# Kernel tuning notes

Measured on AMD Instinct MI355X. Metric: run time of the kernel, lower is better.

## Reference

```python
import jax, jax.numpy as jnp
import numpy as np

N = 100_000      # nodes
E = 1_600_000    # edges (no self loops; reference appends them)
G = 1_000        # graphs
FIN = 27         # input node features
HID = 128        # hidden_channels
L = 4            # num_layers
H = 8            # num_heads
B = 4            # num_bases
A = 3            # aggregators: sum, mean, max
FH = HID // H    # per-head out dim
EPS = 1e-5


def setup_inputs() -> dict:
    key = jax.random.key(0)
    ks = jax.random.split(key, 16)
    s = 0.05
    x = jax.random.normal(ks[0], (N, FIN), jnp.float32)
    src = jax.random.randint(ks[1], (E,), 0, N)
    off = jax.random.randint(ks[2], (E,), 1, N)
    dst = (src + off) % N  # guaranteed no self loops
    edge_index = jnp.stack([src, dst]).astype(jnp.int64)
    batch = jnp.sort(jax.random.randint(ks[3], (N,), 0, G)).astype(jnp.int64)
    return {
        "x": x,
        "lin1_w": jax.random.normal(ks[4], (FIN, HID), jnp.float32) * s,
        "lin1_b": jnp.zeros((HID,), jnp.float32),
        "bn1_g": jnp.ones((HID,), jnp.float32),
        "bn1_b": jnp.zeros((HID,), jnp.float32),
        "bases_w": jax.random.normal(ks[5], (L, HID, B * FH), jnp.float32) * s,
        "comb_w": jax.random.normal(ks[6], (L, HID, H * B * A), jnp.float32) * s,
        "comb_b": jnp.zeros((L, H * B * A), jnp.float32),
        "conv_bias": jnp.zeros((L, HID), jnp.float32),
        "bn_g": jnp.ones((L, HID), jnp.float32),
        "bn_b": jnp.zeros((L, HID), jnp.float32),
        "mlp_w1": jax.random.normal(ks[7], (HID, HID // 2), jnp.float32) * s,
        "mbn1_g": jnp.ones((HID // 2,), jnp.float32),
        "mbn1_b": jnp.zeros((HID // 2,), jnp.float32),
        "mlp_w2": jax.random.normal(ks[8], (HID // 2, HID // 4), jnp.float32) * s,
        "mbn2_g": jnp.ones((HID // 4,), jnp.float32),
        "mbn2_b": jnp.zeros((HID // 4,), jnp.float32),
        "mlp_w3": jax.random.normal(ks[9], (HID // 4, 10), jnp.float32) * s,
        "mlp_b3": jnp.zeros((10,), jnp.float32),
        "edge_index": edge_index,
        "batch": batch,
    }


def _bn(h, g, b):
    # BatchNorm1d, training mode (biased batch variance), per-feature over nodes
    mu = jnp.mean(h, axis=0)
    var = jnp.mean((h - mu) ** 2, axis=0)
    return g * (h - mu) * jax.lax.rsqrt(var + EPS) + b


def reference(x, lin1_w, lin1_b, bn1_g, bn1_b, bases_w, comb_w, comb_b,
              conv_bias, bn_g, bn_b, mlp_w1, mbn1_g, mbn1_b, mlp_w2,
              mbn2_g, mbn2_b, mlp_w3, mlp_b3, edge_index, batch):
    # add self loops (inputs contain none, matching remove+add in EGConv)
    loop = jnp.arange(N, dtype=edge_index.dtype)
    src = jnp.concatenate([edge_index[0], loop])
    dst = jnp.concatenate([edge_index[1], loop])

    h = jax.nn.relu(_bn(x @ lin1_w + lin1_b, bn1_g, bn1_b))  # [N, HID]

    ones_e = jnp.ones((src.shape[0], 1), h.dtype)
    deg = jax.ops.segment_sum(ones_e, dst, num_segments=N)  # [N,1], >=1 via self loops

    for l in range(L):
        bases = h @ bases_w[l]                              # [N, B*FH]
        comb = (h @ comb_w[l] + comb_b[l]).reshape(N, H, A * B)
        msg = bases[src]                                    # [E+N, B*FH]
        ssum = jax.ops.segment_sum(msg, dst, num_segments=N)
        smean = ssum / deg
        smax = jax.ops.segment_max(msg, dst, num_segments=N)
        agg = jnp.stack([ssum, smean, smax], axis=1)        # [N, A, B*FH]
        agg = agg.reshape(N, A * B, FH)
        out = jnp.einsum('nhk,nkf->nhf', comb, agg).reshape(N, HID) + conv_bias[l]
        h = h + jax.nn.relu(_bn(out, bn_g[l], bn_b[l]))

    # global mean pool over graphs
    gsum = jax.ops.segment_sum(h, batch, num_segments=G)
    gcnt = jnp.maximum(jax.ops.segment_sum(jnp.ones((N, 1), h.dtype), batch, num_segments=G), 1.0)
    g = gsum / gcnt                                         # [G, HID]

    g = jax.nn.relu(_bn(g @ mlp_w1, mbn1_g, mbn1_b))
    g = jax.nn.relu(_bn(g @ mlp_w2, mbn2_g, mbn2_b))
    return g @ mlp_w3 + mlp_b3                              # [G, 10]
```

## Files before the change

kernel.cpp:

```cpp
#include <hip/hip_runtime.h>

#define EPSV 1e-5f
#define NEGINF -3.402823466e38f
#define NBMAX 1600
#define CHUNK 8192
#define CAP3 6144

typedef short bf16x8 __attribute__((ext_vector_type(8)));
typedef float f32x4 __attribute__((ext_vector_type(4)));

__device__ __forceinline__ unsigned short f2bf(float f) {
    union { float f; unsigned i; } c; c.f = f;
    unsigned r = c.i + 0x7fff + ((c.i >> 16) & 1);
    return (unsigned short)(r >> 16);
}
__device__ __forceinline__ float blo(unsigned u) {
    union { unsigned i; float f; } c; c.i = u << 16; return c.f;
}
__device__ __forceinline__ float bhi(unsigned u) {
    union { unsigned i; float f; } c; c.i = u & 0xffff0000u; return c.f;
}

__global__ void k_lin1(const float* __restrict__ x, const float* __restrict__ w,
                       const float* __restrict__ bvec, float* __restrict__ outb,
                       float* __restrict__ stats, int N)
{
    int l  = threadIdx.x & 63;
    int wv = threadIdx.x >> 6;
    int waveSlots = gridDim.x * 4;
    int trips = (N + waveSlots - 1) / waveSlots;
    float s0 = 0.f, q0 = 0.f, s1 = 0.f, q1 = 0.f;
    for (int it = 0; it < trips; ++it) {
        int n = (it * gridDim.x + blockIdx.x) * 4 + wv;
        if (n < N) {
            const float* xr = x + (size_t)n * 27;
            float a0 = bvec[l], a1 = bvec[64 + l];
            #pragma unroll
            for (int k = 0; k < 27; ++k) {
                float xv = xr[k];
                a0 = fmaf(xv, w[k * 128 + l], a0);
                a1 = fmaf(xv, w[k * 128 + 64 + l], a1);
            }
            outb[(size_t)n * 128 + l] = a0;
            outb[(size_t)n * 128 + 64 + l] = a1;
            s0 += a0; q0 += a0 * a0; s1 += a1; q1 += a1 * a1;
        }
    }
    __shared__ float sred[4][256];
    sred[0][threadIdx.x] = s0; sred[1][threadIdx.x] = q0;
    sred[2][threadIdx.x] = s1; sred[3][threadIdx.x] = q1;
    __syncthreads();
    if (threadIdx.x < 64) {
        int t = threadIdx.x;
        float v0 = sred[0][t] + sred[0][t + 64] + sred[0][t + 128] + sred[0][t + 192];
        float v1 = sred[1][t] + sred[1][t + 64] + sred[1][t + 128] + sred[1][t + 192];
        float v2 = sred[2][t] + sred[2][t + 64] + sred[2][t + 128] + sred[2][t + 192];
        float v3 = sred[3][t] + sred[3][t + 64] + sred[3][t + 128] + sred[3][t + 192];
        atomicAdd(stats + t, v0);
        atomicAdd(stats + 128 + t, v1);
        atomicAdd(stats + 64 + t, v2);
        atomicAdd(stats + 192 + t, v3);
    }
}

__global__ __launch_bounds__(256)
void k_p1_hist(const int* __restrict__ dst, int* __restrict__ bcnt,
               int E, int NB, int shift)
{
    __shared__ int hist[NBMAX];
    for (int i = threadIdx.x; i < NB; i += 256) hist[i] = 0;
    __syncthreads();
    int stride = gridDim.x * 256;
    for (int e = blockIdx.x * 256 + threadIdx.x; e < E; e += stride)
        atomicAdd(&hist[dst[e] >> shift], 1);
    __syncthreads();
    for (int i = threadIdx.x; i < NB; i += 256)
        if (hist[i]) atomicAdd(bcnt + i, hist[i]);
}

__global__ void k_scan1(const int* __restrict__ cnt, int* __restrict__ rowptr,
                        int* __restrict__ bsum, int N)
{
    __shared__ int sb[256];
    int i = blockIdx.x * 256 + threadIdx.x;
    int v = (i < N) ? cnt[i] : 0;
    sb[threadIdx.x] = v;
    __syncthreads();
    for (int ofs = 1; ofs < 256; ofs <<= 1) {
        int u = (threadIdx.x >= ofs) ? sb[threadIdx.x - ofs] : 0;
        __syncthreads();
        sb[threadIdx.x] += u;
        __syncthreads();
    }
    if (i < N) rowptr[i] = sb[threadIdx.x] - v;
    if (threadIdx.x == 255) bsum[blockIdx.x] = sb[255];
}

__global__ void k_scan2(int* __restrict__ bs, int nb)
{
    __shared__ int sb[512];
    int t = threadIdx.x;
    int v = (t < nb) ? bs[t] : 0;
    sb[t] = v;
    __syncthreads();
    for (int ofs = 1; ofs < 512; ofs <<= 1) {
        int u = (t >= ofs) ? sb[t - ofs] : 0;
        __syncthreads();
        sb[t] += u;
        __syncthreads();
    }
    bs[t] = sb[t] - v;
}

__global__ void k_scan3(int* __restrict__ rowptr, const int* __restrict__ bsum,
                        int N, int E)
{
    int i = blockIdx.x * blockDim.x + threadIdx.x;
    if (i < N) rowptr[i] += bsum[i >> 8];
    if (i == 0) rowptr[N] = E;
}

__global__ __launch_bounds__(256)
void k_p2_scatter(const int* __restrict__ src, const int* __restrict__ dst,
                  const int* __restrict__ bbase, int* __restrict__ bcur0,
                  uint2* __restrict__ bucketed, int E, int NB, int shift)
{
    __shared__ uint2 ebuf[CHUNK];
    __shared__ int hist[NBMAX];
    __shared__ int cur[NBMAX];
    __shared__ int wtmp[256];
    int tid = threadIdx.x;
    int c0 = blockIdx.x * CHUNK;
    int cc = min(CHUNK, E - c0);
    if (cc <= 0) return;

    for (int i = tid; i < NB; i += 256) hist[i] = 0;
    __syncthreads();
    for (int i = tid; i < cc; i += 256)
        atomicAdd(&hist[dst[c0 + i] >> shift], 1);
    __syncthreads();
    int per = (NB + 255) / 256;
    int beg = tid * per, end = min(beg + per, NB);
    int s = 0;
    for (int i = beg; i < end; ++i) s += hist[i];
    wtmp[tid] = s;
    __syncthreads();
    for (int ofs = 1; ofs < 256; ofs <<= 1) {
        int u = (tid >= ofs) ? wtmp[tid - ofs] : 0;
        __syncthreads();
        wtmp[tid] += u;
        __syncthreads();
    }
    int run = wtmp[tid] - s;
    for (int i = beg; i < end; ++i) { cur[i] = run; run += hist[i]; }
    __syncthreads();
    for (int i = tid; i < cc; i += 256) {
        int sv = src[c0 + i], dv = dst[c0 + i];
        int b = dv >> shift;
        int pos = atomicAdd(&cur[b], 1);
        ebuf[pos] = make_uint2((unsigned)sv, (unsigned)dv);
    }
    __syncthreads();
    for (int b = tid; b < NB; b += 256) {
        int c = hist[b];
        if (c > 0) {
            int lb = cur[b] - c;
            int gb = bbase[b] + atomicAdd(&bcur0[b], c);
            hist[b] = gb - lb;
        }
    }
    __syncthreads();
    for (int i = tid; i < cc; i += 256) {
        uint2 u = ebuf[i];
        int b = (int)(u.y >> shift);
        bucketed[hist[b] + i] = u;
    }
}

__global__ __launch_bounds__(256)
void k_p3_csr(const uint2* __restrict__ bucketed, const int* __restrict__ bbase,
              int* __restrict__ rowptr, int* __restrict__ csr,
              int N, int NB, int shift)
{
    __shared__ int ncnt[128], nsc[128];
    __shared__ int lcsr[CAP3];
    int b = blockIdx.x;
    int tid = threadIdx.x;
    int e0 = bbase[b], e1 = bbase[b + 1];
    int cnt = e1 - e0;
    int node0 = b << shift;
    int nodes = min(1 << shift, N - node0);

    if (tid < 128) ncnt[tid] = 0;
    __syncthreads();
    for (int i = tid; i < cnt; i += 256)
        atomicAdd(&ncnt[(int)bucketed[e0 + i].y - node0], 1);
    __syncthreads();
    if (tid < 128) nsc[tid] = ncnt[tid];
    __syncthreads();
    for (int ofs = 1; ofs < 128; ofs <<= 1) {
        int u = 0;
        if (tid < 128 && tid >= ofs) u = nsc[tid - ofs];
        __syncthreads();
        if (tid < 128) nsc[tid] += u;
        __syncthreads();
    }
    if (tid < nodes) rowptr[node0 + tid] = e0 + nsc[tid] - ncnt[tid];
    if (tid == 0 && b == NB - 1) rowptr[N] = e1;
    if (tid < 128) ncnt[tid] = nsc[tid] - ncnt[tid];
    __syncthreads();
    if (cnt <= CAP3) {
        for (int i = tid; i < cnt; i += 256) {
            uint2 u = bucketed[e0 + i];
            int d = (int)u.y - node0;
            int pos = atomicAdd(&ncnt[d], 1);
            lcsr[pos] = (int)u.x;
        }
        __syncthreads();
        for (int i = tid; i < cnt; i += 256) csr[e0 + i] = lcsr[i];
    } else {
        for (int i = tid; i < cnt; i += 256) {
            uint2 u = bucketed[e0 + i];
            int d = (int)u.y - node0;
            int pos = atomicAdd(&ncnt[d], 1);
            csr[e0 + pos] = (int)u.x;
        }
    }
}

__global__ __launch_bounds__(256)
void k_gemm_mfma(const float* __restrict__ tin, float* __restrict__ h,
                 const float* __restrict__ stats, const float* __restrict__ gamma,
                 const float* __restrict__ beta, float invN, int residual,
                 const float* __restrict__ basesW, const float* __restrict__ combW,
                 const float* __restrict__ combB,
                 unsigned short* __restrict__ basesP,
                 unsigned short* __restrict__ combB16, int N)
{
    __shared__ unsigned short Wlds[2560 * 8];
    __shared__ float scL[128], shL[128];
    int tid = threadIdx.x;
    if (tid < 128) {
        float mu  = stats[tid] * invN;
        float var = stats[128 + tid] * invN - mu * mu;
        float sc  = gamma[tid] * rsqrtf(var + EPSV);
        scL[tid] = sc;
        shL[tid] = beta[tid] - mu * sc;
    }
    for (int i = tid; i < 2560; i += 256) {
        int ct = i >> 8, rem = i & 255;
        int ln = rem & 63;
        int n16 = ln & 15, quad = ln >> 4;
        int k = ((rem >> 6) << 5) + quad * 8;
        unsigned short tmp[8];
        if (ct < 4) {
            int c = ct * 16 + n16;
            #pragma unroll
            for (int j = 0; j < 8; ++j) tmp[j] = f2bf(basesW[(k + j) * 64 + c]);
        } else {
            int c = (ct - 4) * 16 + n16;
            #pragma unroll
            for (int j = 0; j < 8; ++j) tmp[j] = f2bf(combW[(k + j) * 96 + c]);
        }
        uint4 pk;
        pk.x = (unsigned)tmp[0] | ((unsigned)tmp[1] << 16);
        pk.y = (unsigned)tmp[2] | ((unsigned)tmp[3] << 16);
        pk.z = (unsigned)tmp[4] | ((unsigned)tmp[5] << 16);
        pk.w = (unsigned)tmp[6] | ((unsigned)tmp[7] << 16);
        *(uint4*)&Wlds[(size_t)i * 8] = pk;
    }
    __syncthreads();

    int lane = tid & 63, wv = tid >> 6;
    int f = lane & 15, quad = lane >> 4;
    float cbv[6];
    #pragma unroll
    for (int s = 0; s < 6; ++s) cbv[s] = combB[s * 16 + f];

    int tiles = (N + 15) >> 4;
    int waveSlots = gridDim.x * 4;
    for (int tile = blockIdx.x * 4 + wv; tile < tiles; tile += waveSlots) {
        int tb = tile * 16;
        int mnode = min(tb + f, N - 1);
        size_t rbase = (size_t)mnode * 128;

        f32x4 acc[10];
        #pragma unroll
        for (int ct = 0; ct < 10; ++ct) acc[ct] = (f32x4){0.f, 0.f, 0.f, 0.f};

        #pragma unroll
        for (int ki = 0; ki < 4; ++ki) {
            int kc = quad * 8 + ki * 32;
            float4 t0 = *(const float4*)&tin[rbase + kc];
            float4 t1 = *(const float4*)&tin[rbase + kc + 4];
            float4 r0, r1;
            r0.x = fmaxf(t0.x * scL[kc]     + shL[kc],     0.f);
            r0.y = fmaxf(t0.y * scL[kc + 1] + shL[kc + 1], 0.f);
            r0.z = fmaxf(t0.z * scL[kc + 2] + shL[kc + 2], 0.f);
            r0.w = fmaxf(t0.w * scL[kc + 3] + shL[kc + 3], 0.f);
            r1.x = fmaxf(t1.x * scL[kc + 4] + shL[kc + 4], 0.f);
            r1.y = fmaxf(t1.y * scL[kc + 5] + shL[kc + 5], 0.f);
            r1.z = fmaxf(t1.z * scL[kc + 6] + shL[kc + 6], 0.f);
            r1.w = fmaxf(t1.w * scL[kc + 7] + shL[kc + 7], 0.f);
            if (residual) {
                float4 h0 = *(const float4*)&h[rbase + kc];
                float4 h1 = *(const float4*)&h[rbase + kc + 4];
                r0.x += h0.x; r0.y += h0.y; r0.z += h0.z; r0.w += h0.w;
                r1.x += h1.x; r1.y += h1.y; r1.z += h1.z; r1.w += h1.w;
            }
            *(float4*)&h[rbase + kc] = r0;
            *(float4*)&h[rbase + kc + 4] = r1;
            short ab[8];
            ab[0] = (short)f2bf(r0.x); ab[1] = (short)f2bf(r0.y);
            ab[2] = (short)f2bf(r0.z); ab[3] = (short)f2bf(r0.w);
            ab[4] = (short)f2bf(r1.x); ab[5] = (short)f2bf(r1.y);
            ab[6] = (short)f2bf(r1.z); ab[7] = (short)f2bf(r1.w);
            bf16x8 a = *(bf16x8*)ab;
            #pragma unroll
            for (int ct = 0; ct < 10; ++ct) {
                bf16x8 bfr = *(const bf16x8*)&Wlds[(size_t)((ct * 4 + ki) * 64 + lane) * 8];
                acc[ct] = __builtin_amdgcn_mfma_f32_16x16x32_bf16(a, bfr, acc[ct], 0, 0, 0);
            }
        }

        #pragma unroll
        for (int r = 0; r < 4; ++r) {
            int node = tb + quad * 4 + r;
            if (node < N) {
                #pragma unroll
                for (int ct = 0; ct < 4; ++ct)
                    basesP[(size_t)node * 64 + f * 4 + ct] = f2bf(acc[ct][r]);
                #pragma unroll
                for (int s = 0; s < 6; ++s)
                    combB16[(size_t)node * 96 + s * 16 + f] = f2bf(acc[4 + s][r] + cbv[s]);
            }
        }
    }
}

__global__ __launch_bounds__(256)
void k_agg(const uint2* __restrict__ basesP2, const unsigned short* __restrict__ combB16,
           const int* __restrict__ csr, const int* __restrict__ rowptr,
           const float* __restrict__ cbias, float* __restrict__ outb,
           float* __restrict__ stats, int N)
{
    int l = threadIdx.x & 63;
    int w = threadIdx.x >> 6;
    int f = l & 15, sub = l >> 4;
    int waveSlots = gridDim.x * 4;
    int trips = (N + waveSlots - 1) / waveSlots;
    float s0 = 0.f, q0 = 0.f, s1 = 0.f, q1 = 0.f;

    for (int it = 0; it < trips; ++it) {
        int n = (it * gridDim.x + blockIdx.x) * 4 + w;
        if (n < N) {
            int row0 = rowptr[n], row1 = rowptr[n + 1];
            int cnt = row1 - row0;
            float S0 = 0.f, S1 = 0.f, S2 = 0.f, S3 = 0.f;
            float M0 = NEGINF, M1 = NEGINF, M2 = NEGINF, M3 = NEGINF;
            int j = 0;
            while (j < cnt) {
                int chunk = min(64, cnt - j);
                int idx = (l < chunk) ? csr[row0 + j + l] : 0;
                int full = chunk >> 2;
                int t = 0;
                #pragma unroll 4
                for (; t < full; ++t) {
                    int sn = __shfl(idx, 4 * t + sub, 64);
                    uint2 u = basesP2[(size_t)sn * 16 + f];
                    float v0 = blo(u.x), v1 = bhi(u.x), v2 = blo(u.y), v3 = bhi(u.y);
                    S0 += v0; S1 += v1; S2 += v2; S3 += v3;
                    M0 = fmaxf(M0, v0); M1 = fmaxf(M1, v1);
                    M2 = fmaxf(M2, v2); M3 = fmaxf(M3, v3);
                }
                int nG = (chunk + 3) >> 2;
                for (; t < nG; ++t) {
                    int e = 4 * t + sub;
                    int sn = __shfl(idx, min(e, chunk - 1), 64);
                    uint2 u = basesP2[(size_t)sn * 16 + f];
                    if (e < chunk) {
                        float v0 = blo(u.x), v1 = bhi(u.x), v2 = blo(u.y), v3 = bhi(u.y);
                        S0 += v0; S1 += v1; S2 += v2; S3 += v3;
                        M0 = fmaxf(M0, v0); M1 = fmaxf(M1, v1);
                        M2 = fmaxf(M2, v2); M3 = fmaxf(M3, v3);
                    }
                }
                j += chunk;
            }
            S0 += __shfl_xor(S0, 16, 64); S1 += __shfl_xor(S1, 16, 64);
            S2 += __shfl_xor(S2, 16, 64); S3 += __shfl_xor(S3, 16, 64);
            S0 += __shfl_xor(S0, 32, 64); S1 += __shfl_xor(S1, 32, 64);
            S2 += __shfl_xor(S2, 32, 64); S3 += __shfl_xor(S3, 32, 64);
            M0 = fmaxf(M0, __shfl_xor(M0, 16, 64)); M1 = fmaxf(M1, __shfl_xor(M1, 16, 64));
            M2 = fmaxf(M2, __shfl_xor(M2, 16, 64)); M3 = fmaxf(M3, __shfl_xor(M3, 16, 64));
            M0 = fmaxf(M0, __shfl_xor(M0, 32, 64)); M1 = fmaxf(M1, __shfl_xor(M1, 32, 64));
            M2 = fmaxf(M2, __shfl_xor(M2, 32, 64)); M3 = fmaxf(M3, __shfl_xor(M3, 32, 64));
            uint2 su = basesP2[(size_t)n * 16 + f];
            float w0 = blo(su.x), w1 = bhi(su.x), w2 = blo(su.y), w3 = bhi(su.y);
            S0 += w0; S1 += w1; S2 += w2; S3 += w3;
            M0 = fmaxf(M0, w0); M1 = fmaxf(M1, w1);
            M2 = fmaxf(M2, w2); M3 = fmaxf(M3, w3);
            float invd = 1.f / (float)(cnt + 1);
            float A0 = S0 * invd, A1 = S1 * invd, A2 = S2 * invd, A3 = S3 * invd;

            const unsigned short* cr = combB16 + (size_t)n * 96;
            const uint2* c0p = (const uint2*)(cr + sub * 12);
            const uint2* c1p = (const uint2*)(cr + 48 + sub * 12);
            uint2 qa0 = c0p[0], qa1 = c0p[1], qa2 = c0p[2];
            uint2 qb0 = c1p[0], qb1 = c1p[1], qb2 = c1p[2];

            float o0 = cbias[l], o1 = cbias[64 + l];
            o0 = fmaf(blo(qa0.x), S0, o0); o0 = fmaf(bhi(qa0.x), S1, o0);
            o0 = fmaf(blo(qa0.y), S2, o0); o0 = fmaf(bhi(qa0.y), S3, o0);
            o0 = fmaf(blo(qa1.x), A0, o0); o0 = fmaf(bhi(qa1.x), A1, o0);
            o0 = fmaf(blo(qa1.y), A2, o0); o0 = fmaf(bhi(qa1.y), A3, o0);
            o0 = fmaf(blo(qa2.x), M0, o0); o0 = fmaf(bhi(qa2.x), M1, o0);
            o0 = fmaf(blo(qa2.y), M2, o0); o0 = fmaf(bhi(qa2.y), M3, o0);
            o1 = fmaf(blo(qb0.x), S0, o1); o1 = fmaf(bhi(qb0.x), S1, o1);
            o1 = fmaf(blo(qb0.y), S2, o1); o1 = fmaf(bhi(qb0.y), S3, o1);
            o1 = fmaf(blo(qb1.x), A0, o1); o1 = fmaf(bhi(qb1.x), A1, o1);
            o1 = fmaf(blo(qb1.y), A2, o1); o1 = fmaf(bhi(qb1.y), A3, o1);
            o1 = fmaf(blo(qb2.x), M0, o1); o1 = fmaf(bhi(qb2.x), M1, o1);
            o1 = fmaf(blo(qb2.y), M2, o1); o1 = fmaf(bhi(qb2.y), M3, o1);

            outb[(size_t)n * 128 + l] = o0;
            outb[(size_t)n * 128 + 64 + l] = o1;
            s0 += o0; q0 += o0 * o0; s1 += o1; q1 += o1 * o1;
        }
    }
    __shared__ float sred[4][256];
    sred[0][threadIdx.x] = s0; sred[1][threadIdx.x] = q0;
    sred[2][threadIdx.x] = s1; sred[3][threadIdx.x] = q1;
    __syncthreads();
    if (threadIdx.x < 64) {
        int t = threadIdx.x;
        float v0 = sred[0][t] + sred[0][t + 64] + sred[0][t + 128] + sred[0][t + 192];
        float v1 = sred[1][t] + sred[1][t + 64] + sred[1][t + 128] + sred[1][t + 192];
        float v2 = sred[2][t] + sred[2][t + 64] + sred[2][t + 128] + sred[2][t + 192];
        float v3 = sred[3][t] + sred[3][t + 64] + sred[3][t + 128] + sred[3][t + 192];
        atomicAdd(stats + t, v0);
        atomicAdd(stats + 128 + t, v1);
        atomicAdd(stats + 64 + t, v2);
        atomicAdd(stats + 192 + t, v3);
    }
}

__global__ void k_gbound(const int* __restrict__ batch, int* __restrict__ gstart,
                         int N, int G)
{
    int stride = gridDim.x * blockDim.x;
    for (int n = blockIdx.x * blockDim.x + threadIdx.x; n < N; n += stride) {
        int b = batch[n];
        if (n == 0) {
            for (int g = 0; g <= b; ++g) gstart[g] = 0;
        } else {
            int pb = batch[n - 1];
            for (int g = pb + 1; g <= b; ++g) gstart[g] = n;
        }
        if (n == N - 1) {
            for (int g = b + 1; g <= G; ++g) gstart[g] = N;
        }
    }
}

__global__ void k_gmean(const float* __restrict__ t, const float* __restrict__ h,
                        const float* __restrict__ stats, const float* __restrict__ gamma,
                        const float* __restrict__ beta, float invN,
                        const int* __restrict__ gstart, float* __restrict__ gout, int G)
{
    int g = blockIdx.x;
    if (g >= G) return;
    int c = threadIdx.x;
    float mu  = stats[c] * invN;
    float var = stats[128 + c] * invN - mu * mu;
    float sc  = gamma[c] * rsqrtf(var + EPSV);
    float sh  = beta[c] - mu * sc;
    int s = gstart[g], e = gstart[g + 1];
    float acc = 0.f;
    for (int n = s; n < e; ++n) {
        size_t o = (size_t)n * 128 + c;
        acc += h[o] + fmaxf(t[o] * sc + sh, 0.f);
    }
    float cntf = fmaxf((float)(e - s), 1.f);
    gout[g * 128 + c] = acc / cntf;
}

__global__ void k_mlp1(const float* __restrict__ gin, const float* __restrict__ w1,
                       float* __restrict__ t1, float* __restrict__ stats, int G)
{
    int g = blockIdx.x;
    int c = threadIdx.x;
    const float* gr = gin + g * 128;
    float acc = 0.f;
    for (int k = 0; k < 128; ++k) acc = fmaf(gr[k], w1[k * 64 + c], acc);
    t1[g * 64 + c] = acc;
    atomicAdd(stats + c, acc);
    atomicAdd(stats + 64 + c, acc * acc);
}

__global__ void k_mlp2(const float* __restrict__ t1, const float* __restrict__ stats1,
                       const float* __restrict__ g1, const float* __restrict__ b1,
                       const float* __restrict__ w2, float* __restrict__ t2,
                       float* __restrict__ stats2, float invG, int G)
{
    __shared__ float row[64];
    int g = blockIdx.x;
    int c = threadIdx.x;
    float v = t1[g * 64 + c];
    float mu = stats1[c] * invG;
    float var = stats1[64 + c] * invG - mu * mu;
    row[c] = fmaxf(g1[c] * (v - mu) * rsqrtf(var + EPSV) + b1[c], 0.f);
    __syncthreads();
    if (c < 32) {
        float acc = 0.f;
        #pragma unroll
        for (int k = 0; k < 64; ++k) acc = fmaf(row[k], w2[k * 32 + c], acc);
        t2[g * 32 + c] = acc;
        atomicAdd(stats2 + c, acc);
        atomicAdd(stats2 + 32 + c, acc * acc);
    }
}

__global__ void k_mlp3(const float* __restrict__ t2, const float* __restrict__ stats2,
                       const float* __restrict__ g2, const float* __restrict__ b2,
                       const float* __restrict__ w3, const float* __restrict__ b3,
                       float* __restrict__ out, float invG, int G)
{
    __shared__ float row[32];
    int g = blockIdx.x;
    int c = threadIdx.x;
    if (c < 32) {
        float v = t2[g * 32 + c];
        float mu = stats2[c] * invG;
        float var = stats2[32 + c] * invG - mu * mu;
        row[c] = fmaxf(g2[c] * (v - mu) * rsqrtf(var + EPSV) + b2[c], 0.f);
    }
    __syncthreads();
    if (c < 10) {
        float acc = b3[c];
        #pragma unroll
        for (int k = 0; k < 32; ++k) acc = fmaf(row[k], w3[k * 10 + c], acc);
        out[g * 10 + c] = acc;
    }
}

extern "C" void kernel_launch(void* const* d_in, const int* in_sizes, int n_in,
                              void* d_out, int out_size, void* d_ws, size_t ws_size,
                              hipStream_t stream)
{
    const float* x        = (const float*)d_in[0];
    const float* lin1_w   = (const float*)d_in[1];
    const float* lin1_b   = (const float*)d_in[2];
    const float* bn1_g    = (const float*)d_in[3];
    const float* bn1_b    = (const float*)d_in[4];
    const float* bases_w  = (const float*)d_in[5];
    const float* comb_w   = (const float*)d_in[6];
    const float* comb_b   = (const float*)d_in[7];
    const float* conv_bias= (const float*)d_in[8];
    const float* bn_g     = (const float*)d_in[9];
    const float* bn_b     = (const float*)d_in[10];
    const float* mlp_w1   = (const float*)d_in[11];
    const float* mbn1_g   = (const float*)d_in[12];
    const float* mbn1_b   = (const float*)d_in[13];
    const float* mlp_w2   = (const float*)d_in[14];
    const float* mbn2_g   = (const float*)d_in[15];
    const float* mbn2_b   = (const float*)d_in[16];
    const float* mlp_w3   = (const float*)d_in[17];
    const float* mlp_b3   = (const float*)d_in[18];
    const int*   edge_idx = (const int*)d_in[19];
    const int*   batch    = (const int*)d_in[20];
    float* outp = (float*)d_out;

    const int N = in_sizes[20];
    const int E = in_sizes[19] / 2;
    const int G = out_size / 10;
    const int* esrc = edge_idx;
    const int* edst = edge_idx + E;

    int shift = 6;
    while ((((N - 1) >> shift) + 1) > NBMAX && shift < 7) ++shift;
    const int NB = ((N - 1) >> shift) + 1;

    char* p = (char*)d_ws;
    auto alloc = [&](size_t bytes) {
        char* r = p;
        p += (bytes + 255) & ~(size_t)255;
        return r;
    };
    float*          h      = (float*)alloc((size_t)N * 128 * 4);
    unsigned short* basesP = (unsigned short*)alloc((size_t)N * 64 * 2);
    unsigned short* combB16= (unsigned short*)alloc((size_t)N * 96 * 2);
    float*          outb   = (float*)alloc((size_t)N * 128 * 4);
    int*            csr    = (int*)  alloc((size_t)E * 4);
    int*            rowptr = (int*)  alloc((size_t)(N + 1) * 4);
    int*            bbase  = (int*)  alloc((size_t)(NB + 1) * 4);
    float*          tg     = (float*)alloc((size_t)G * 128 * 4);
    float*          t1     = (float*)alloc((size_t)G * 64 * 4);
    float*          t2     = (float*)alloc((size_t)G * 32 * 4);
    int*            gstart = (int*)  alloc((size_t)(G + 1) * 4);
    int*            bsum   = (int*)  alloc(512 * 4);
    char*           zbase  = p;
    int*            bcnt   = (int*)  alloc((size_t)NB * 4);
    int*            bcur0  = (int*)  alloc((size_t)NB * 4);
    float*          stats  = (float*)alloc(7 * 256 * 4);
    size_t zbytes = (size_t)(p - zbase);
    uint2* bucketed = (uint2*)combB16;
    (void)ws_size; (void)n_in;

    hipMemsetAsync(zbase, 0, zbytes, stream);

    const float invN = 1.0f / (float)N;
    const float invG = 1.0f / (float)G;
    const int nbB = (NB + 255) / 256;

    k_lin1<<<1024, 256, 0, stream>>>(x, lin1_w, lin1_b, outb, stats, N);
    k_p1_hist<<<256, 256, 0, stream>>>(edst, bcnt, E, NB, shift);
    k_scan1<<<nbB, 256, 0, stream>>>(bcnt, bbase, bsum, NB);
    k_scan2<<<1, 512, 0, stream>>>(bsum, nbB);
    k_scan3<<<nbB, 256, 0, stream>>>(bbase, bsum, NB, E);
    k_p2_scatter<<<(E + CHUNK - 1) / CHUNK, 256, 0, stream>>>(esrc, edst, bbase, bcur0,
                                                              bucketed, E, NB, shift);
    k_p3_csr<<<NB, 256, 0, stream>>>(bucketed, bbase, rowptr, csr, N, NB, shift);

    for (int l = 0; l < 4; ++l) {
        const float* bw = bases_w + (size_t)l * 128 * 64;
        const float* cw = comb_w + (size_t)l * 128 * 96;
        const float* cb = comb_b + (size_t)l * 96;
        const float* cvb = conv_bias + (size_t)l * 128;
        const float* pg = (l == 0) ? bn1_g : bn_g + (l - 1) * 128;
        const float* pb = (l == 0) ? bn1_b : bn_b + (l - 1) * 128;
        k_gemm_mfma<<<512, 256, 0, stream>>>(outb, h, stats + l * 256, pg, pb, invN,
                                             l > 0 ? 1 : 0, bw, cw, cb, basesP, combB16, N);
        k_agg<<<2048, 256, 0, stream>>>((const uint2*)basesP, combB16, csr, rowptr, cvb,
                                        outb, stats + (1 + l) * 256, N);
    }

    k_gbound<<<512, 256, 0, stream>>>(batch, gstart, N, G);
    k_gmean<<<G, 128, 0, stream>>>(outb, h, stats + 4 * 256, bn_g + 3 * 128,
                                   bn_b + 3 * 128, invN, gstart, tg, G);
    float* st5 = stats + 5 * 256;
    float* st6 = stats + 6 * 256;
    k_mlp1<<<G, 64, 0, stream>>>(tg, mlp_w1, t1, st5, G);
    k_mlp2<<<G, 64, 0, stream>>>(t1, st5, mbn1_g, mbn1_b, mlp_w2, t2, st6, invG, G);
    k_mlp3<<<G, 64, 0, stream>>>(t2, st6, mbn2_g, mbn2_b, mlp_w3, mlp_b3, outp, invG, G);
}
```

Before: 864.0 us.

## Stage lin1 weights in LDS, simplify agg gather, split gmean rows

k_lin1 now copies its 27x128 weight matrix into shared memory once per block and hoists the bias loads. k_agg drops the chunked csr load plus shuffle broadcast and instead has each lane read its neighbour index directly from csr. It also uses 32-bit byte-offset addressing into the bf16 bases buffer and hoists the conv bias loads. k_gmean runs 256 threads per graph, with two halves accumulating alternate nodes and combining through shared memory, to get more parallelism. The direct csr loads add redundant per-lane index traffic, and the 32-bit offsets assume the buffer stays under 4GB.

```diff
diff --git a/kernel.cpp b/kernel.cpp
--- a/kernel.cpp
+++ b/kernel.cpp
@@ -21,12 +21,19 @@
     union { unsigned i; float f; } c; c.i = u & 0xffff0000u; return c.f;
 }
 
-__global__ void k_lin1(const float* __restrict__ x, const float* __restrict__ w,
-                       const float* __restrict__ bvec, float* __restrict__ outb,
-                       float* __restrict__ stats, int N)
-{
-    int l  = threadIdx.x & 63;
-    int wv = threadIdx.x >> 6;
+__global__ __launch_bounds__(256)
+void k_lin1(const float* __restrict__ x, const float* __restrict__ w,
+            const float* __restrict__ bvec, float* __restrict__ outb,
+            float* __restrict__ stats, int N)
+{
+    __shared__ float wl[27 * 128];
+    int tid = threadIdx.x;
+    for (int i = tid; i < 27 * 128; i += 256) wl[i] = w[i];
+    __syncthreads();
+
+    int l  = tid & 63;
+    int wv = tid >> 6;
+    float bv0 = bvec[l], bv1 = bvec[64 + l];
     int waveSlots = gridDim.x * 4;
     int trips = (N + waveSlots - 1) / waveSlots;
     float s0 = 0.f, q0 = 0.f, s1 = 0.f, q1 = 0.f;
@@ -34,12 +41,12 @@
         int n = (it * gridDim.x + blockIdx.x) * 4 + wv;
         if (n < N) {
             const float* xr = x + (size_t)n * 27;
-            float a0 = bvec[l], a1 = bvec[64 + l];
+            float a0 = bv0, a1 = bv1;
             #pragma unroll
             for (int k = 0; k < 27; ++k) {
                 float xv = xr[k];
-                a0 = fmaf(xv, w[k * 128 + l], a0);
-                a1 = fmaf(xv, w[k * 128 + 64 + l], a1);
+                a0 = fmaf(xv, wl[k * 128 + l], a0);
+                a1 = fmaf(xv, wl[k * 128 + 64 + l], a1);
             }
             outb[(size_t)n * 128 + l] = a0;
             outb[(size_t)n * 128 + 64 + l] = a1;
@@ -47,11 +54,11 @@
         }
     }
     __shared__ float sred[4][256];
-    sred[0][threadIdx.x] = s0; sred[1][threadIdx.x] = q0;
-    sred[2][threadIdx.x] = s1; sred[3][threadIdx.x] = q1;
-    __syncthreads();
-    if (threadIdx.x < 64) {
-        int t = threadIdx.x;
+    sred[0][tid] = s0; sred[1][tid] = q0;
+    sred[2][tid] = s1; sred[3][tid] = q1;
+    __syncthreads();
+    if (tid < 64) {
+        int t = tid;
         float v0 = sred[0][t] + sred[0][t + 64] + sred[0][t + 128] + sred[0][t + 192];
         float v1 = sred[1][t] + sred[1][t + 64] + sred[1][t + 128] + sred[1][t + 192];
         float v2 = sred[2][t] + sred[2][t + 64] + sred[2][t + 128] + sred[2][t + 192];
@@ -339,7 +346,7 @@
 }
 
 __global__ __launch_bounds__(256)
-void k_agg(const uint2* __restrict__ basesP2, const unsigned short* __restrict__ combB16,
+void k_agg(const unsigned short* __restrict__ basesP, const unsigned short* __restrict__ combB16,
            const int* __restrict__ csr, const int* __restrict__ rowptr,
            const float* __restrict__ cbias, float* __restrict__ outb,
            float* __restrict__ stats, int N)
@@ -347,6 +354,9 @@
     int l = threadIdx.x & 63;
     int w = threadIdx.x >> 6;
     int f = l & 15, sub = l >> 4;
+    const char* bp = (const char*)basesP;
+    unsigned fof = (unsigned)(f << 3);
+    float cb0 = cbias[l], cb1 = cbias[64 + l];
     int waveSlots = gridDim.x * 4;
     int trips = (N + waveSlots - 1) / waveSlots;
     float s0 = 0.f, q0 = 0.f, s1 = 0.f, q1 = 0.f;
@@ -358,34 +368,28 @@
             int cnt = row1 - row0;
             float S0 = 0.f, S1 = 0.f, S2 = 0.f, S3 = 0.f;
             float M0 = NEGINF, M1 = NEGINF, M2 = NEGINF, M3 = NEGINF;
-            int j = 0;
-            while (j < cnt) {
-                int chunk = min(64, cnt - j);
-                int idx = (l < chunk) ? csr[row0 + j + l] : 0;
-                int full = chunk >> 2;
-                int t = 0;
-                #pragma unroll 4
-                for (; t < full; ++t) {
-                    int sn = __shfl(idx, 4 * t + sub, 64);
-                    uint2 u = basesP2[(size_t)sn * 16 + f];
+            const int* cs = csr + row0 + sub;
+            int tfull = cnt >> 2;
+            #pragma unroll 4
+            for (int t = 0; t < tfull; ++t) {
+                int sn = cs[4 * t];
+                uint2 u = *(const uint2*)(bp + (((unsigned)sn) << 7) + fof);
+                float v0 = blo(u.x), v1 = bhi(u.x), v2 = blo(u.y), v3 = bhi(u.y);
+                S0 += v0; S1 += v1; S2 += v2; S3 += v3;
+                M0 = fmaxf(M0, v0); M1 = fmaxf(M1, v1);
+                M2 = fmaxf(M2, v2); M3 = fmaxf(M3, v3);
+            }
+            int rem = cnt & 3;
+            if (rem) {
+                int e = (cnt & ~3) + sub;
+                int sn = csr[row0 + min(e, cnt - 1)];
+                uint2 u = *(const uint2*)(bp + (((unsigned)sn) << 7) + fof);
+                if (sub < rem) {
                     float v0 = blo(u.x), v1 = bhi(u.x), v2 = blo(u.y), v3 = bhi(u.y);
                     S0 += v0; S1 += v1; S2 += v2; S3 += v3;
                     M0 = fmaxf(M0, v0); M1 = fmaxf(M1, v1);
                     M2 = fmaxf(M2, v2); M3 = fmaxf(M3, v3);
                 }
-                int nG = (chunk + 3) >> 2;
-                for (; t < nG; ++t) {
-                    int e = 4 * t + sub;
-                    int sn = __shfl(idx, min(e, chunk - 1), 64);
-                    uint2 u = basesP2[(size_t)sn * 16 + f];
-                    if (e < chunk) {
-                        float v0 = blo(u.x), v1 = bhi(u.x), v2 = blo(u.y), v3 = bhi(u.y);
-                        S0 += v0; S1 += v1; S2 += v2; S3 += v3;
-                        M0 = fmaxf(M0, v0); M1 = fmaxf(M1, v1);
-                        M2 = fmaxf(M2, v2); M3 = fmaxf(M3, v3);
-                    }
-                }
-                j += chunk;
             }
             S0 += __shfl_xor(S0, 16, 64); S1 += __shfl_xor(S1, 16, 64);
             S2 += __shfl_xor(S2, 16, 64); S3 += __shfl_xor(S3, 16, 64);
@@ -395,7 +399,7 @@
             M2 = fmaxf(M2, __shfl_xor(M2, 16, 64)); M3 = fmaxf(M3, __shfl_xor(M3, 16, 64));
             M0 = fmaxf(M0, __shfl_xor(M0, 32, 64)); M1 = fmaxf(M1, __shfl_xor(M1, 32, 64));
             M2 = fmaxf(M2, __shfl_xor(M2, 32, 64)); M3 = fmaxf(M3, __shfl_xor(M3, 32, 64));
-            uint2 su = basesP2[(size_t)n * 16 + f];
+            uint2 su = *(const uint2*)(bp + (((unsigned)n) << 7) + fof);
             float w0 = blo(su.x), w1 = bhi(su.x), w2 = blo(su.y), w3 = bhi(su.y);
             S0 += w0; S1 += w1; S2 += w2; S3 += w3;
             M0 = fmaxf(M0, w0); M1 = fmaxf(M1, w1);
@@ -409,7 +413,7 @@
             uint2 qa0 = c0p[0], qa1 = c0p[1], qa2 = c0p[2];
             uint2 qb0 = c1p[0], qb1 = c1p[1], qb2 = c1p[2];
 
-            float o0 = cbias[l], o1 = cbias[64 + l];
+            float o0 = cb0, o1 = cb1;
             o0 = fmaf(blo(qa0.x), S0, o0); o0 = fmaf(bhi(qa0.x), S1, o0);
             o0 = fmaf(blo(qa0.y), S2, o0); o0 = fmaf(bhi(qa0.y), S3, o0);
             o0 = fmaf(blo(qa1.x), A0, o0); o0 = fmaf(bhi(qa1.x), A1, o0);
@@ -463,26 +467,35 @@
     }
 }
 
-__global__ void k_gmean(const float* __restrict__ t, const float* __restrict__ h,
-                        const float* __restrict__ stats, const float* __restrict__ gamma,
-                        const float* __restrict__ beta, float invN,
-                        const int* __restrict__ gstart, float* __restrict__ gout, int G)
-{
+__global__ __launch_bounds__(256)
+void k_gmean(const float* __restrict__ t, const float* __restrict__ h,
+             const float* __restrict__ stats, const float* __restrict__ gamma,
+             const float* __restrict__ beta, float invN,
+             const int* __restrict__ gstart, float* __restrict__ gout, int G)
+{
+    __shared__ float part[128];
     int g = blockIdx.x;
     if (g >= G) return;
-    int c = threadIdx.x;
+    int c = threadIdx.x & 127;
+    int half = threadIdx.x >> 7;
     float mu  = stats[c] * invN;
     float var = stats[128 + c] * invN - mu * mu;
     float sc  = gamma[c] * rsqrtf(var + EPSV);
     float sh  = beta[c] - mu * sc;
     int s = gstart[g], e = gstart[g + 1];
     float acc = 0.f;
-    for (int n = s; n < e; ++n) {
+    #pragma unroll 2
+    for (int n = s + half; n < e; n += 2) {
         size_t o = (size_t)n * 128 + c;
         acc += h[o] + fmaxf(t[o] * sc + sh, 0.f);
     }
-    float cntf = fmaxf((float)(e - s), 1.f);
-    gout[g * 128 + c] = acc / cntf;
+    if (half) part[c] = acc;
+    __syncthreads();
+    if (!half) {
+        float tot = acc + part[c];
+        float cntf = fmaxf((float)(e - s), 1.f);
+        gout[g * 128 + c] = tot / cntf;
+    }
 }
 
 __global__ void k_mlp1(const float* __restrict__ gin, const float* __restrict__ w1,
@@ -631,12 +644,12 @@
         const float* pb = (l == 0) ? bn1_b : bn_b + (l - 1) * 128;
         k_gemm_mfma<<<512, 256, 0, stream>>>(outb, h, stats + l * 256, pg, pb, invN,
                                              l > 0 ? 1 : 0, bw, cw, cb, basesP, combB16, N);
-        k_agg<<<2048, 256, 0, stream>>>((const uint2*)basesP, combB16, csr, rowptr, cvb,
+        k_agg<<<2048, 256, 0, stream>>>(basesP, combB16, csr, rowptr, cvb,
                                         outb, stats + (1 + l) * 256, N);
     }
 
     k_gbound<<<512, 256, 0, stream>>>(batch, gstart, N, G);
-    k_gmean<<<G, 128, 0, stream>>>(outb, h, stats + 4 * 256, bn_g + 3 * 128,
+    k_gmean<<<G, 256, 0, stream>>>(outb, h, stats + 4 * 256, bn_g + 3 * 128,
                                    bn_b + 3 * 128, invN, gstart, tg, G);
     float* st5 = stats + 5 * 256;
     float* st6 = stats + 6 * 256;
```

After: 818.1 us. 1.06x faster.
